# Kernel tuning notes

Hardware: AMD Instinct MI355X
Metric: run time of the kernel (lower is better)

## Reference

```python
import jax, jax.numpy as jnp
import numpy as np

N = 4096
IN_DIM = 256
OUT_DIM = 256
NUM_HEADS = 4
HEAD_DIM = OUT_DIM // NUM_HEADS


def setup_inputs() -> dict:
    key = jax.random.key(0)
    ks = jax.random.split(key, 10)
    x = jax.random.normal(ks[0], (N, IN_DIM), dtype=jnp.float32)
    adj = jax.random.randint(ks[1], (N, N), 0, 2, dtype=jnp.int32)
    adj = jnp.maximum(adj, jnp.eye(N, dtype=jnp.int32))  # self-loops -> no empty rows
    s_in = 1.0 / np.sqrt(IN_DIM)
    s_out = 1.0 / np.sqrt(OUT_DIM)
    Wq = jax.random.uniform(ks[2], (IN_DIM, OUT_DIM), jnp.float32, -s_in, s_in)
    bq = jnp.zeros((OUT_DIM,), jnp.float32)
    Wk = jax.random.uniform(ks[3], (IN_DIM, OUT_DIM), jnp.float32, -s_in, s_in)
    bk = jnp.zeros((OUT_DIM,), jnp.float32)
    Wv = jax.random.uniform(ks[4], (IN_DIM, OUT_DIM), jnp.float32, -s_in, s_in)
    bv = jnp.zeros((OUT_DIM,), jnp.float32)
    Wo = jax.random.uniform(ks[5], (OUT_DIM, OUT_DIM), jnp.float32, -s_out, s_out)
    bo = jnp.zeros((OUT_DIM,), jnp.float32)
    gamma = jnp.ones((OUT_DIM,), jnp.float32)
    beta = jnp.zeros((OUT_DIM,), jnp.float32)
    return {"x": x, "adj": adj, "Wq": Wq, "bq": bq, "Wk": Wk, "bk": bk,
            "Wv": Wv, "bv": bv, "Wo": Wo, "bo": bo, "gamma": gamma, "beta": beta}


def layer_norm(h, gamma, beta, eps=1e-5):
    mu = jnp.mean(h, axis=-1, keepdims=True)
    var = jnp.mean(jnp.square(h - mu), axis=-1, keepdims=True)
    return (h - mu) * jax.lax.rsqrt(var + eps) * gamma + beta


def reference(x, adj, Wq, bq, Wk, bk, Wv, bv, Wo, bo, gamma, beta):
    n = x.shape[0]
    q_proj = x @ Wq + bq                       # (N, out_dim), reused for residual
    Q = q_proj.reshape(n, NUM_HEADS, HEAD_DIM)
    K = (x @ Wk + bk).reshape(n, NUM_HEADS, HEAD_DIM)
    V = (x @ Wv + bv).reshape(n, NUM_HEADS, HEAD_DIM)
    scores = jnp.einsum('nhd,mhd->nmh', Q, K) / np.sqrt(HEAD_DIM)
    scores = jnp.where(adj[:, :, None] == 0, -jnp.inf, scores)
    attn = jax.nn.softmax(scores, axis=1)      # softmax over neighbor axis m
    out = jnp.einsum('nmh,mhd->nhd', attn, V).reshape(n, OUT_DIM)
    out = out @ Wo + bo
    return layer_norm(out + q_proj, gamma, beta)
```

## Files before the change

kernel.cpp:

```cpp
#include <hip/hip_runtime.h>
#include <math.h>

#define NN 4096
#define DIM 256
#define NHEADS 4
#define HDIM 64

typedef short bf16x8 __attribute__((ext_vector_type(8)));
typedef float f32x4  __attribute__((ext_vector_type(4)));

__device__ __forceinline__ unsigned short f2bf(float f) {
    unsigned int u = __float_as_uint(f);
    u += 0x7fffu + ((u >> 16) & 1u);
    return (unsigned short)(u >> 16);
}
__device__ __forceinline__ float bf2f(unsigned short h) {
    return __uint_as_float(((unsigned int)h) << 16);
}
__device__ __forceinline__ void async16(const void* g, void* l) {
    __builtin_amdgcn_global_load_lds(
        (const __attribute__((address_space(1))) unsigned int*)g,
        (__attribute__((address_space(3))) unsigned int*)l, 16, 0, 0);
}

__global__ __launch_bounds__(256)
void prep_kernel(const float* __restrict__ W0, const float* __restrict__ W1,
                 const float* __restrict__ W2, const float* __restrict__ W3,
                 unsigned short* __restrict__ T0, unsigned short* __restrict__ T1,
                 unsigned short* __restrict__ T2, unsigned short* __restrict__ T3)
{
    __shared__ unsigned short Ts[64][65];
    const int b = blockIdx.x, t = threadIdx.x;
    const int mat = b >> 4, tile = b & 15;
    const int r0 = (tile >> 2) * 64, c0 = (tile & 3) * 64;
    const float* W = (mat == 0) ? W0 : (mat == 1) ? W1 : (mat == 2) ? W2 : W3;
    unsigned short* T = (mat == 0) ? T0 : (mat == 1) ? T1 : (mat == 2) ? T2 : T3;
    {
        int r = t >> 2, c4 = (t & 3) * 16;
        #pragma unroll
        for (int j = 0; j < 4; ++j) {
            float4 v = *reinterpret_cast<const float4*>(W + (size_t)(r0 + r) * DIM + c0 + c4 + j * 4);
            Ts[c4 + j * 4 + 0][r] = f2bf(v.x);
            Ts[c4 + j * 4 + 1][r] = f2bf(v.y);
            Ts[c4 + j * 4 + 2][r] = f2bf(v.z);
            Ts[c4 + j * 4 + 3][r] = f2bf(v.w);
        }
    }
    __syncthreads();
    {
        int d = t >> 2, k4 = (t & 3) * 16;
        #pragma unroll
        for (int j = 0; j < 4; ++j) {
            ushort4 u;
            u.x = Ts[d][k4 + j * 4 + 0];
            u.y = Ts[d][k4 + j * 4 + 1];
            u.z = Ts[d][k4 + j * 4 + 2];
            u.w = Ts[d][k4 + j * 4 + 3];
            *reinterpret_cast<ushort4*>(T + (size_t)(c0 + d) * DIM + r0 + k4 + j * 4) = u;
        }
    }
}

__global__ __launch_bounds__(256)
void qkv_mask(const float* __restrict__ x,
              const unsigned short* __restrict__ WqT, const unsigned short* __restrict__ WkT,
              const unsigned short* __restrict__ WvT,
              const float* __restrict__ bq, const float* __restrict__ bk, const float* __restrict__ bv,
              unsigned short* __restrict__ Qo, unsigned short* __restrict__ Ko,
              unsigned short* __restrict__ VTo,
              const int* __restrict__ adj, unsigned long long* __restrict__ maskT)
{
    const int b = blockIdx.x, t = threadIdx.x, w = t >> 6, l = t & 63;

    if (b >= 384) {
        const int ww = (b - 384) * 4 + w;
        for (int idx = ww; idx < 65536; idx += 8192) {
            const int row = idx >> 4, st = idx & 15;
            const int4 a = *reinterpret_cast<const int4*>(adj + (size_t)row * NN + st * 256 + l * 4);
            unsigned long long b0 = __ballot(a.x != 0);
            unsigned long long b1 = __ballot(a.y != 0);
            unsigned long long b2 = __ballot(a.z != 0);
            unsigned long long b3 = __ballot(a.w != 0);
            if (l < 4) {
                unsigned long long bb = (l == 0) ? b0 : (l == 1) ? b1 : (l == 2) ? b2 : b3;
                maskT[(size_t)row * 64 + st * 4 + l] = bb;
            }
        }
        return;
    }

    const int l15 = l & 15, lg = l >> 4;
    const int which = b >> 7, xb = b & 127;
    const int row0 = xb * 32 + (w >> 1) * 16;
    const int col0 = (w & 1) * 128;
    const unsigned short* WT; const float* bias;
    if (which == 0)      { WT = WqT; bias = bq; }
    else if (which == 1) { WT = WkT; bias = bk; }
    else                 { WT = WvT; bias = bv; }

    f32x4 acc[8] = {};
    for (int k0 = 0; k0 < DIM; k0 += 32) {
        const float* xp = x + (size_t)(row0 + l15) * DIM + k0 + lg * 8;
        float4 x0 = *reinterpret_cast<const float4*>(xp);
        float4 x1 = *reinterpret_cast<const float4*>(xp + 4);
        union { unsigned u[4]; bf16x8 v; } xa;
        asm("v_cvt_pk_bf16_f32 %0, %1, %2" : "=v"(xa.u[0]) : "v"(x0.x), "v"(x0.y));
        asm("v_cvt_pk_bf16_f32 %0, %1, %2" : "=v"(xa.u[1]) : "v"(x0.z), "v"(x0.w));
        asm("v_cvt_pk_bf16_f32 %0, %1, %2" : "=v"(xa.u[2]) : "v"(x1.x), "v"(x1.y));
        asm("v_cvt_pk_bf16_f32 %0, %1, %2" : "=v"(xa.u[3]) : "v"(x1.z), "v"(x1.w));
        #pragma unroll
        for (int nt = 0; nt < 8; ++nt) {
            bf16x8 wb = *(const bf16x8*)(WT + (size_t)(col0 + nt * 16 + l15) * DIM + k0 + lg * 8);
            acc[nt] = __builtin_amdgcn_mfma_f32_16x16x32_bf16(xa.v, wb, acc[nt], 0, 0, 0);
        }
    }
    #pragma unroll
    for (int nt = 0; nt < 8; ++nt) {
        int col = col0 + nt * 16 + l15;
        float bb = bias[col];
        #pragma unroll
        for (int r = 0; r < 4; ++r) {
            int row = row0 + lg * 4 + r;
            unsigned short val = f2bf(acc[nt][r] + bb);
            if (which == 2) {
                int rb = row & 63;
                int vnt = rb >> 4, vlg = (rb >> 2) & 3, vr = rb & 3;
                int pos = ((vnt & 1) << 5) | (vlg << 3) | ((vnt >> 1) << 2) | vr;
                VTo[(size_t)col * NN + ((row & ~63) | pos)] = val;
            } else if (which == 0) Qo[(size_t)row * DIM + col] = val;
            else                   Ko[(size_t)row * DIM + col] = val;
        }
    }
}

template<int NTILES>
__global__ __launch_bounds__(256)
void attn_mfma(const unsigned short* __restrict__ Qb, const unsigned short* __restrict__ Kb,
               const unsigned short* __restrict__ VT, const unsigned long long* __restrict__ maskT,
               unsigned short* __restrict__ Opart, float* __restrict__ lpart)
{
    constexpr int NSTR = NTILES / 4;
    __shared__ unsigned short Kt[2][64][64];
    __shared__ unsigned short Vt[2][64][64];

    const int t = threadIdx.x, w = t >> 6, l = t & 63, l15 = l & 15, lg = l >> 4;
    const int n0 = blockIdx.x * 128, h = blockIdx.y, sp = blockIdx.z;
    const int kv_base = sp * NTILES * 64;
    const int qbase = n0 + w * 32;

    bf16x8 qa[2][2];
    #pragma unroll
    for (int sub = 0; sub < 2; ++sub) {
        const unsigned short* qp = Qb + (size_t)(qbase + sub * 16 + l15) * DIM + h * HDIM + lg * 8;
        qa[sub][0] = *(const bf16x8*)(qp);
        qa[sub][1] = *(const bf16x8*)(qp + 32);
    }

    const unsigned long long* mbase0 = maskT + (size_t)(qbase + l15) * 64 + (kv_base >> 6);
    const unsigned long long* mbase1 = maskT + (size_t)(qbase + 16 + l15) * 64 + (kv_base >> 6);

    const int srow  = w * 16 + (l >> 3);
    const int sunit = (l & 7) ^ (srow & 7);
    const unsigned short* kS = Kb + (size_t)(kv_base + srow) * DIM + h * HDIM + sunit * 8;
    const unsigned short* vS = VT + (size_t)(h * HDIM + srow) * NN + kv_base + sunit * 8;

    const int xr  = l15 & 7;
    const int ko0 = (lg ^ xr) << 4;
    const int ko1 = ((4 + lg) ^ xr) << 4;

    f32x4 oa[2][4] = {};
    float lsum[2] = {0.f, 0.f};

    {
        unsigned short* kd = &Kt[0][w * 16][0];
        unsigned short* vd = &Vt[0][w * 16][0];
        async16(kS,           kd);
        async16(kS + 8 * DIM, kd + 8 * 64);
        async16(vS,           vd);
        async16(vS + 8 * NN,  vd + 8 * 64);
    }

    #pragma unroll
    for (int st = 0; st < NSTR; ++st) {
        ulonglong4 m40 = *reinterpret_cast<const ulonglong4*>(mbase0 + st * 4);
        ulonglong4 m41 = *reinterpret_cast<const ulonglong4*>(mbase1 + st * 4);
        unsigned lo[2][4], hi[2][4];
        lo[0][0] = (unsigned)m40.x; hi[0][0] = (unsigned)(m40.x >> 32);
        lo[0][1] = (unsigned)m40.y; hi[0][1] = (unsigned)(m40.y >> 32);
        lo[0][2] = (unsigned)m40.z; hi[0][2] = (unsigned)(m40.z >> 32);
        lo[0][3] = (unsigned)m40.w; hi[0][3] = (unsigned)(m40.w >> 32);
        lo[1][0] = (unsigned)m41.x; hi[1][0] = (unsigned)(m41.x >> 32);
        lo[1][1] = (unsigned)m41.y; hi[1][1] = (unsigned)(m41.y >> 32);
        lo[1][2] = (unsigned)m41.z; hi[1][2] = (unsigned)(m41.z >> 32);
        lo[1][3] = (unsigned)m41.w; hi[1][3] = (unsigned)(m41.w >> 32);

        #pragma unroll
        for (int m = 0; m < 4; ++m) {
            const int tl = st * 4 + m;
            const int bsel = tl & 1;
            if (tl + 1 < NTILES) {
                const unsigned short* ks = kS + (size_t)(tl + 1) * 64 * DIM;
                const unsigned short* vs = vS + (tl + 1) * 64;
                unsigned short* kd = &Kt[bsel ^ 1][w * 16][0];
                unsigned short* vd = &Vt[bsel ^ 1][w * 16][0];
                async16(ks,           kd);
                async16(ks + 8 * DIM, kd + 8 * 64);
                async16(vs,           vd);
                async16(vs + 8 * NN,  vd + 8 * 64);
                asm volatile("s_waitcnt vmcnt(4)" ::: "memory");
            } else {
                asm volatile("s_waitcnt vmcnt(0)" ::: "memory");
            }
            __builtin_amdgcn_s_barrier();
            __builtin_amdgcn_sched_barrier(0);

            const char* kbase = (const char*)&Kt[bsel][0][0] + l15 * 128;
            const char* vbase = (const char*)&Vt[bsel][0][0] + l15 * 128;

            f32x4 sa[2][4] = {};
            __builtin_amdgcn_s_setprio(1);
            #pragma unroll
            for (int nt = 0; nt < 4; ++nt) {
                bf16x8 kb0 = *(const bf16x8*)(kbase + nt * 2048 + ko0);
                bf16x8 kb1 = *(const bf16x8*)(kbase + nt * 2048 + ko1);
                #pragma unroll
                for (int sub = 0; sub < 2; ++sub) {
                    sa[sub][nt] = __builtin_amdgcn_mfma_f32_16x16x32_bf16(kb0, qa[sub][0], sa[sub][nt], 0, 0, 0);
                    sa[sub][nt] = __builtin_amdgcn_mfma_f32_16x16x32_bf16(kb1, qa[sub][1], sa[sub][nt], 0, 0, 0);
                }
            }
            __builtin_amdgcn_s_setprio(0);

            const int bsh = ((m & 1) << 4) + lg;
            bf16x8 pa[2][2];
            #pragma unroll
            for (int sub = 0; sub < 2; ++sub) {
                unsigned s0 = ((m & 2) ? hi[sub][0] : lo[sub][0]) >> bsh;
                unsigned s1 = ((m & 2) ? hi[sub][1] : lo[sub][1]) >> bsh;
                unsigned s2 = ((m & 2) ? hi[sub][2] : lo[sub][2]) >> bsh;
                unsigned s3 = ((m & 2) ? hi[sub][3] : lo[sub][3]) >> bsh;
                float p[4][4];
                #pragma unroll
                for (int nt = 0; nt < 4; ++nt) {
                    p[nt][0] = exp2f(((s0 >> (nt * 4)) & 1u) ? sa[sub][nt][0] * 0.18033688f : -INFINITY);
                    p[nt][1] = exp2f(((s1 >> (nt * 4)) & 1u) ? sa[sub][nt][1] * 0.18033688f : -INFINITY);
                    p[nt][2] = exp2f(((s2 >> (nt * 4)) & 1u) ? sa[sub][nt][2] * 0.18033688f : -INFINITY);
                    p[nt][3] = exp2f(((s3 >> (nt * 4)) & 1u) ? sa[sub][nt][3] * 0.18033688f : -INFINITY);
                }
                lsum[sub] += (((p[0][0] + p[0][1]) + (p[0][2] + p[0][3])) +
                              ((p[1][0] + p[1][1]) + (p[1][2] + p[1][3]))) +
                             (((p[2][0] + p[2][1]) + (p[2][2] + p[2][3])) +
                              ((p[3][0] + p[3][1]) + (p[3][2] + p[3][3])));
                union { unsigned u[4]; bf16x8 v; } a0, a1;
                asm("v_cvt_pk_bf16_f32 %0, %1, %2" : "=v"(a0.u[0]) : "v"(p[0][0]), "v"(p[0][1]));
                asm("v_cvt_pk_bf16_f32 %0, %1, %2" : "=v"(a0.u[1]) : "v"(p[0][2]), "v"(p[0][3]));
                asm("v_cvt_pk_bf16_f32 %0, %1, %2" : "=v"(a0.u[2]) : "v"(p[2][0]), "v"(p[2][1]));
                asm("v_cvt_pk_bf16_f32 %0, %1, %2" : "=v"(a0.u[3]) : "v"(p[2][2]), "v"(p[2][3]));
                asm("v_cvt_pk_bf16_f32 %0, %1, %2" : "=v"(a1.u[0]) : "v"(p[1][0]), "v"(p[1][1]));
                asm("v_cvt_pk_bf16_f32 %0, %1, %2" : "=v"(a1.u[1]) : "v"(p[1][2]), "v"(p[1][3]));
                asm("v_cvt_pk_bf16_f32 %0, %1, %2" : "=v"(a1.u[2]) : "v"(p[3][0]), "v"(p[3][1]));
                asm("v_cvt_pk_bf16_f32 %0, %1, %2" : "=v"(a1.u[3]) : "v"(p[3][2]), "v"(p[3][3]));
                pa[sub][0] = a0.v;
                pa[sub][1] = a1.v;
            }

            __builtin_amdgcn_s_setprio(1);
            #pragma unroll
            for (int nt = 0; nt < 4; ++nt) {
                bf16x8 vb0 = *(const bf16x8*)(vbase + nt * 2048 + ko0);
                bf16x8 vb1 = *(const bf16x8*)(vbase + nt * 2048 + ko1);
                #pragma unroll
                for (int sub = 0; sub < 2; ++sub) {
                    oa[sub][nt] = __builtin_amdgcn_mfma_f32_16x16x32_bf16(pa[sub][0], vb0, oa[sub][nt], 0, 0, 0);
                    oa[sub][nt] = __builtin_amdgcn_mfma_f32_16x16x32_bf16(pa[sub][1], vb1, oa[sub][nt], 0, 0, 0);
                }
            }
            __builtin_amdgcn_s_setprio(0);

            __builtin_amdgcn_sched_barrier(0);
            __builtin_amdgcn_s_barrier();
        }
    }

    #pragma unroll
    for (int sub = 0; sub < 2; ++sub) {
        float v = lsum[sub];
        v += __shfl_xor(v, 16);
        v += __shfl_xor(v, 32);
        if (lg == 0)
            lpart[((size_t)sp * NN + qbase + sub * 16 + l15) * NHEADS + h] = v;
        #pragma unroll
        for (int r = 0; r < 4; ++r) {
            const int qr = qbase + sub * 16 + lg * 4 + r;
            #pragma unroll
            for (int nt = 0; nt < 4; ++nt)
                Opart[((size_t)sp * NN + qr) * DIM + h * HDIM + nt * 16 + l15] = f2bf(oa[sub][nt][r]);
        }
    }
}

__global__ __launch_bounds__(256)
void combine_kernel(const unsigned short* __restrict__ Opart, const float* __restrict__ lpart,
                    unsigned short* __restrict__ AOb, int S)
{
    const int tid = blockIdx.x * blockDim.x + threadIdx.x;
    const int q  = tid >> 6;
    const int d  = (tid & 63) * 4;
    const int h  = d >> 6;
    float o0 = 0.f, o1 = 0.f, o2 = 0.f, o3 = 0.f, lsum = 0.f;
    for (int s = 0; s < S; ++s) {
        ushort4 u = *reinterpret_cast<const ushort4*>(Opart + ((size_t)s * NN + q) * DIM + d);
        o0 += bf2f(u.x); o1 += bf2f(u.y); o2 += bf2f(u.z); o3 += bf2f(u.w);
        lsum += lpart[((size_t)s * NN + q) * NHEADS + h];
    }
    float inv = 1.f / lsum;
    ushort4 o;
    o.x = f2bf(o0 * inv); o.y = f2bf(o1 * inv); o.z = f2bf(o2 * inv); o.w = f2bf(o3 * inv);
    *reinterpret_cast<ushort4*>(AOb + (size_t)q * DIM + d) = o;
}

__global__ __launch_bounds__(256)
void out_ln(const unsigned short* __restrict__ Ab, const unsigned short* __restrict__ WoT,
            const float* __restrict__ bo, const unsigned short* __restrict__ Rb,
            const float* __restrict__ gamma, const float* __restrict__ beta,
            float* __restrict__ out)
{
    __shared__ float redsum[4][16];
    __shared__ float redsq[4][16];
    const int t = threadIdx.x, w = t >> 6, l = t & 63, l15 = l & 15, lg = l >> 4;
    const int row0 = blockIdx.x * 16;
    const int col0 = w * 64;

    f32x4 acc[4] = {};
    for (int k0 = 0; k0 < DIM; k0 += 32) {
        bf16x8 xa = *(const bf16x8*)(Ab + (size_t)(row0 + l15) * DIM + k0 + lg * 8);
        #pragma unroll
        for (int nt = 0; nt < 4; ++nt) {
            bf16x8 wb = *(const bf16x8*)(WoT + (size_t)(col0 + nt * 16 + l15) * DIM + k0 + lg * 8);
            acc[nt] = __builtin_amdgcn_mfma_f32_16x16x32_bf16(xa, wb, acc[nt], 0, 0, 0);
        }
    }

    float psum[4] = {0, 0, 0, 0}, psq[4] = {0, 0, 0, 0};
    #pragma unroll
    for (int nt = 0; nt < 4; ++nt) {
        int col = col0 + nt * 16 + l15;
        float bb = bo[col];
        #pragma unroll
        for (int r = 0; r < 4; ++r) {
            int row = row0 + lg * 4 + r;
            float xv = acc[nt][r] + bb + bf2f(Rb[(size_t)row * DIM + col]);
            acc[nt][r] = xv;
            psum[r] += xv; psq[r] += xv * xv;
        }
    }
    #pragma unroll
    for (int r = 0; r < 4; ++r) {
        float s = psum[r], q = psq[r];
        s += __shfl_xor(s, 1); q += __shfl_xor(q, 1);
        s += __shfl_xor(s, 2); q += __shfl_xor(q, 2);
        s += __shfl_xor(s, 4); q += __shfl_xor(q, 4);
        s += __shfl_xor(s, 8); q += __shfl_xor(q, 8);
        psum[r] = s; psq[r] = q;
    }
    if (l15 == 0) {
        #pragma unroll
        for (int r = 0; r < 4; ++r) {
            redsum[w][lg * 4 + r] = psum[r];
            redsq[w][lg * 4 + r]  = psq[r];
        }
    }
    __syncthreads();

    float msave[4], rsave[4];
    #pragma unroll
    for (int r = 0; r < 4; ++r) {
        int row = lg * 4 + r;
        float s = redsum[0][row] + redsum[1][row] + redsum[2][row] + redsum[3][row];
        float q = redsq[0][row] + redsq[1][row] + redsq[2][row] + redsq[3][row];
        float mean = s * (1.f / 256.f);
        float var  = q * (1.f / 256.f) - mean * mean;
        msave[r] = mean;
        rsave[r] = rsqrtf(var + 1e-5f);
    }
    #pragma unroll
    for (int nt = 0; nt < 4; ++nt) {
        int col = col0 + nt * 16 + l15;
        float g = gamma[col], bt = beta[col];
        #pragma unroll
        for (int r = 0; r < 4; ++r) {
            int row = row0 + lg * 4 + r;
            out[(size_t)row * DIM + col] = (acc[nt][r] - msave[r]) * rsave[r] * g + bt;
        }
    }
}

extern "C" void kernel_launch(void* const* d_in, const int* in_sizes, int n_in,
                              void* d_out, int out_size, void* d_ws, size_t ws_size,
                              hipStream_t stream) {
    const float* x     = (const float*)d_in[0];
    const int*   adj   = (const int*)  d_in[1];
    const float* Wq    = (const float*)d_in[2];
    const float* bq    = (const float*)d_in[3];
    const float* Wk    = (const float*)d_in[4];
    const float* bk    = (const float*)d_in[5];
    const float* Wv    = (const float*)d_in[6];
    const float* bv    = (const float*)d_in[7];
    const float* Wo    = (const float*)d_in[8];
    const float* bo    = (const float*)d_in[9];
    const float* gamma = (const float*)d_in[10];
    const float* beta  = (const float*)d_in[11];
    float* out = (float*)d_out;

    char* ws = (char*)d_ws;
    const size_t MB = 1u << 20;
    unsigned short*     Qb    = (unsigned short*)(ws + 0 * MB);
    unsigned short*     Kb    = (unsigned short*)(ws + 2 * MB);
    unsigned short*     VT    = (unsigned short*)(ws + 4 * MB);
    unsigned long long* maskT = (unsigned long long*)(ws + 6 * MB);
    unsigned short*     WqT   = (unsigned short*)(ws + 8 * MB);
    unsigned short*     WkT   = (unsigned short*)(ws + 8 * MB + 128 * 1024);
    unsigned short*     WvT   = (unsigned short*)(ws + 8 * MB + 256 * 1024);
    unsigned short*     WoT   = (unsigned short*)(ws + 8 * MB + 384 * 1024);
    unsigned short*     AOb   = (unsigned short*)(ws + 8 * MB + 512 * 1024);
    float*              lpart = (float*)(ws + 10 * MB + 512 * 1024);
    unsigned short*     Opart = (unsigned short*)(ws + 11 * MB);

    const int S = (ws_size >= 27 * MB) ? 8 : 4;

    prep_kernel<<<64, 256, 0, stream>>>(Wq, Wk, Wv, Wo, WqT, WkT, WvT, WoT);

    qkv_mask<<<384 + 2048, 256, 0, stream>>>(
        x, WqT, WkT, WvT, bq, bk, bv, Qb, Kb, VT, adj, maskT);

    if (S == 8)
        attn_mfma<8><<<dim3(NN / 128, NHEADS, 8), 256, 0, stream>>>(
            Qb, Kb, VT, maskT, Opart, lpart);
    else
        attn_mfma<16><<<dim3(NN / 128, NHEADS, 4), 256, 0, stream>>>(
            Qb, Kb, VT, maskT, Opart, lpart);

    combine_kernel<<<NN * DIM / 4 / 256, 256, 0, stream>>>(Opart, lpart, AOb, S);

    out_ln<<<NN / 16, 256, 0, stream>>>(AOb, WoT, bo, Qb, gamma, beta, out);
}
```

Baseline: 90.74 us.

## Triple-buffer K/V tiles, halve query rows per block, prescale K

The attention kernel moves from double to triple buffering of K/V tiles in LDS. Prefetch now runs two tiles ahead, with one barrier per tile instead of two. Each wave handles 16 query rows instead of 32, so the grid doubles and register pressure drops, but each block reuses fewer loaded K/V tiles and global K/V traffic doubles. The softmax scale is folded into K when it is stored in the projection kernel, which removes a multiply per score.

```diff
diff --git a/kernel.cpp b/kernel.cpp
--- a/kernel.cpp
+++ b/kernel.cpp
@@ -121,7 +121,9 @@
         #pragma unroll
         for (int r = 0; r < 4; ++r) {
             int row = row0 + lg * 4 + r;
-            unsigned short val = f2bf(acc[nt][r] + bb);
+            float ov = acc[nt][r] + bb;
+            if (which == 1) ov *= 0.18033688f;
+            unsigned short val = f2bf(ov);
             if (which == 2) {
                 int rb = row & 63;
                 int vnt = rb >> 4, vlg = (rb >> 2) & 3, vr = rb & 3;
@@ -140,24 +142,19 @@
                unsigned short* __restrict__ Opart, float* __restrict__ lpart)
 {
     constexpr int NSTR = NTILES / 4;
-    __shared__ unsigned short Kt[2][64][64];
-    __shared__ unsigned short Vt[2][64][64];
+    __shared__ unsigned short Kt[3][64][64];
+    __shared__ unsigned short Vt[3][64][64];
 
     const int t = threadIdx.x, w = t >> 6, l = t & 63, l15 = l & 15, lg = l >> 4;
-    const int n0 = blockIdx.x * 128, h = blockIdx.y, sp = blockIdx.z;
+    const int n0 = blockIdx.x * 64, h = blockIdx.y, sp = blockIdx.z;
     const int kv_base = sp * NTILES * 64;
-    const int qbase = n0 + w * 32;
-
-    bf16x8 qa[2][2];
-    #pragma unroll
-    for (int sub = 0; sub < 2; ++sub) {
-        const unsigned short* qp = Qb + (size_t)(qbase + sub * 16 + l15) * DIM + h * HDIM + lg * 8;
-        qa[sub][0] = *(const bf16x8*)(qp);
-        qa[sub][1] = *(const bf16x8*)(qp + 32);
-    }
-
-    const unsigned long long* mbase0 = maskT + (size_t)(qbase + l15) * 64 + (kv_base >> 6);
-    const unsigned long long* mbase1 = maskT + (size_t)(qbase + 16 + l15) * 64 + (kv_base >> 6);
+    const int qrow = n0 + w * 16;
+
+    const unsigned short* qp = Qb + (size_t)(qrow + l15) * DIM + h * HDIM + lg * 8;
+    const bf16x8 qa0 = *(const bf16x8*)(qp);
+    const bf16x8 qa1 = *(const bf16x8*)(qp + 32);
+
+    const unsigned long long* mbase = maskT + (size_t)(qrow + l15) * 64 + (kv_base >> 6);
 
     const int srow  = w * 16 + (l >> 3);
     const int sunit = (l & 7) ^ (srow & 7);
@@ -168,134 +165,113 @@
     const int ko0 = (lg ^ xr) << 4;
     const int ko1 = ((4 + lg) ^ xr) << 4;
 
-    f32x4 oa[2][4] = {};
-    float lsum[2] = {0.f, 0.f};
-
-    {
-        unsigned short* kd = &Kt[0][w * 16][0];
-        unsigned short* vd = &Vt[0][w * 16][0];
-        async16(kS,           kd);
-        async16(kS + 8 * DIM, kd + 8 * 64);
-        async16(vS,           vd);
-        async16(vS + 8 * NN,  vd + 8 * 64);
+    f32x4 oa[4] = {};
+    float lsum = 0.f;
+
+    #pragma unroll
+    for (int pt = 0; pt < 2; ++pt) {
+        unsigned short* kd = &Kt[pt][w * 16][0];
+        unsigned short* vd = &Vt[pt][w * 16][0];
+        const unsigned short* ks = kS + (size_t)pt * 64 * DIM;
+        const unsigned short* vs = vS + pt * 64;
+        async16(ks, kd); async16(ks + 8 * DIM, kd + 8 * 64);
+        async16(vs, vd); async16(vs + 8 * NN,  vd + 8 * 64);
     }
 
     #pragma unroll
     for (int st = 0; st < NSTR; ++st) {
-        ulonglong4 m40 = *reinterpret_cast<const ulonglong4*>(mbase0 + st * 4);
-        ulonglong4 m41 = *reinterpret_cast<const ulonglong4*>(mbase1 + st * 4);
-        unsigned lo[2][4], hi[2][4];
-        lo[0][0] = (unsigned)m40.x; hi[0][0] = (unsigned)(m40.x >> 32);
-        lo[0][1] = (unsigned)m40.y; hi[0][1] = (unsigned)(m40.y >> 32);
-        lo[0][2] = (unsigned)m40.z; hi[0][2] = (unsigned)(m40.z >> 32);
-        lo[0][3] = (unsigned)m40.w; hi[0][3] = (unsigned)(m40.w >> 32);
-        lo[1][0] = (unsigned)m41.x; hi[1][0] = (unsigned)(m41.x >> 32);
-        lo[1][1] = (unsigned)m41.y; hi[1][1] = (unsigned)(m41.y >> 32);
-        lo[1][2] = (unsigned)m41.z; hi[1][2] = (unsigned)(m41.z >> 32);
-        lo[1][3] = (unsigned)m41.w; hi[1][3] = (unsigned)(m41.w >> 32);
+        const ulonglong4 m4 = *reinterpret_cast<const ulonglong4*>(mbase + st * 4);
+        const unsigned lo[4] = {(unsigned)m4.x, (unsigned)m4.y, (unsigned)m4.z, (unsigned)m4.w};
+        const unsigned hi[4] = {(unsigned)(m4.x >> 32), (unsigned)(m4.y >> 32),
+                                (unsigned)(m4.z >> 32), (unsigned)(m4.w >> 32)};
 
         #pragma unroll
         for (int m = 0; m < 4; ++m) {
             const int tl = st * 4 + m;
-            const int bsel = tl & 1;
-            if (tl + 1 < NTILES) {
-                const unsigned short* ks = kS + (size_t)(tl + 1) * 64 * DIM;
-                const unsigned short* vs = vS + (tl + 1) * 64;
-                unsigned short* kd = &Kt[bsel ^ 1][w * 16][0];
-                unsigned short* vd = &Vt[bsel ^ 1][w * 16][0];
-                async16(ks,           kd);
-                async16(ks + 8 * DIM, kd + 8 * 64);
-                async16(vs,           vd);
-                async16(vs + 8 * NN,  vd + 8 * 64);
-                asm volatile("s_waitcnt vmcnt(4)" ::: "memory");
-            } else {
-                asm volatile("s_waitcnt vmcnt(0)" ::: "memory");
-            }
+            if (tl < NTILES - 1) asm volatile("s_waitcnt vmcnt(4)" ::: "memory");
+            else                 asm volatile("s_waitcnt vmcnt(0)" ::: "memory");
             __builtin_amdgcn_s_barrier();
             __builtin_amdgcn_sched_barrier(0);
 
-            const char* kbase = (const char*)&Kt[bsel][0][0] + l15 * 128;
-            const char* vbase = (const char*)&Vt[bsel][0][0] + l15 * 128;
-
-            f32x4 sa[2][4] = {};
+            if (tl + 2 < NTILES) {
+                const int bb = (tl + 2) % 3;
+                unsigned short* kd = &Kt[bb][w * 16][0];
+                unsigned short* vd = &Vt[bb][w * 16][0];
+                const unsigned short* ks = kS + (size_t)(tl + 2) * 64 * DIM;
+                const unsigned short* vs = vS + (tl + 2) * 64;
+                async16(ks, kd); async16(ks + 8 * DIM, kd + 8 * 64);
+                async16(vs, vd); async16(vs + 8 * NN,  vd + 8 * 64);
+            }
+
+            const int cb = tl % 3;
+            const char* kbase = (const char*)&Kt[cb][0][0] + l15 * 128;
+            const char* vbase = (const char*)&Vt[cb][0][0] + l15 * 128;
+
+            f32x4 sa[4] = {};
             __builtin_amdgcn_s_setprio(1);
             #pragma unroll
             for (int nt = 0; nt < 4; ++nt) {
                 bf16x8 kb0 = *(const bf16x8*)(kbase + nt * 2048 + ko0);
                 bf16x8 kb1 = *(const bf16x8*)(kbase + nt * 2048 + ko1);
-                #pragma unroll
-                for (int sub = 0; sub < 2; ++sub) {
-                    sa[sub][nt] = __builtin_amdgcn_mfma_f32_16x16x32_bf16(kb0, qa[sub][0], sa[sub][nt], 0, 0, 0);
-                    sa[sub][nt] = __builtin_amdgcn_mfma_f32_16x16x32_bf16(kb1, qa[sub][1], sa[sub][nt], 0, 0, 0);
-                }
+                sa[nt] = __builtin_amdgcn_mfma_f32_16x16x32_bf16(kb0, qa0, sa[nt], 0, 0, 0);
+                sa[nt] = __builtin_amdgcn_mfma_f32_16x16x32_bf16(kb1, qa1, sa[nt], 0, 0, 0);
             }
             __builtin_amdgcn_s_setprio(0);
 
             const int bsh = ((m & 1) << 4) + lg;
-            bf16x8 pa[2][2];
+            const unsigned s0 = ((m & 2) ? hi[0] : lo[0]) >> bsh;
+            const unsigned s1 = ((m & 2) ? hi[1] : lo[1]) >> bsh;
+            const unsigned s2 = ((m & 2) ? hi[2] : lo[2]) >> bsh;
+            const unsigned s3 = ((m & 2) ? hi[3] : lo[3]) >> bsh;
+            float p[4][4];
             #pragma unroll
-            for (int sub = 0; sub < 2; ++sub) {
-                unsigned s0 = ((m & 2) ? hi[sub][0] : lo[sub][0]) >> bsh;
-                unsigned s1 = ((m & 2) ? hi[sub][1] : lo[sub][1]) >> bsh;
-                unsigned s2 = ((m & 2) ? hi[sub][2] : lo[sub][2]) >> bsh;
-                unsigned s3 = ((m & 2) ? hi[sub][3] : lo[sub][3]) >> bsh;
-                float p[4][4];
-                #pragma unroll
-                for (int nt = 0; nt < 4; ++nt) {
-                    p[nt][0] = exp2f(((s0 >> (nt * 4)) & 1u) ? sa[sub][nt][0] * 0.18033688f : -INFINITY);
-                    p[nt][1] = exp2f(((s1 >> (nt * 4)) & 1u) ? sa[sub][nt][1] * 0.18033688f : -INFINITY);
-                    p[nt][2] = exp2f(((s2 >> (nt * 4)) & 1u) ? sa[sub][nt][2] * 0.18033688f : -INFINITY);
-                    p[nt][3] = exp2f(((s3 >> (nt * 4)) & 1u) ? sa[sub][nt][3] * 0.18033688f : -INFINITY);
-                }
-                lsum[sub] += (((p[0][0] + p[0][1]) + (p[0][2] + p[0][3])) +
-                              ((p[1][0] + p[1][1]) + (p[1][2] + p[1][3]))) +
-                             (((p[2][0] + p[2][1]) + (p[2][2] + p[2][3])) +
-                              ((p[3][0] + p[3][1]) + (p[3][2] + p[3][3])));
-                union { unsigned u[4]; bf16x8 v; } a0, a1;
-                asm("v_cvt_pk_bf16_f32 %0, %1, %2" : "=v"(a0.u[0]) : "v"(p[0][0]), "v"(p[0][1]));
-                asm("v_cvt_pk_bf16_f32 %0, %1, %2" : "=v"(a0.u[1]) : "v"(p[0][2]), "v"(p[0][3]));
-                asm("v_cvt_pk_bf16_f32 %0, %1, %2" : "=v"(a0.u[2]) : "v"(p[2][0]), "v"(p[2][1]));
-                asm("v_cvt_pk_bf16_f32 %0, %1, %2" : "=v"(a0.u[3]) : "v"(p[2][2]), "v"(p[2][3]));
-                asm("v_cvt_pk_bf16_f32 %0, %1, %2" : "=v"(a1.u[0]) : "v"(p[1][0]), "v"(p[1][1]));
-                asm("v_cvt_pk_bf16_f32 %0, %1, %2" : "=v"(a1.u[1]) : "v"(p[1][2]), "v"(p[1][3]));
-                asm("v_cvt_pk_bf16_f32 %0, %1, %2" : "=v"(a1.u[2]) : "v"(p[3][0]), "v"(p[3][1]));
-                asm("v_cvt_pk_bf16_f32 %0, %1, %2" : "=v"(a1.u[3]) : "v"(p[3][2]), "v"(p[3][3]));
-                pa[sub][0] = a0.v;
-                pa[sub][1] = a1.v;
+            for (int nt = 0; nt < 4; ++nt) {
+                p[nt][0] = exp2f(((s0 >> (nt * 4)) & 1u) ? sa[nt][0] : -INFINITY);
+                p[nt][1] = exp2f(((s1 >> (nt * 4)) & 1u) ? sa[nt][1] : -INFINITY);
+                p[nt][2] = exp2f(((s2 >> (nt * 4)) & 1u) ? sa[nt][2] : -INFINITY);
+                p[nt][3] = exp2f(((s3 >> (nt * 4)) & 1u) ? sa[nt][3] : -INFINITY);
             }
+            lsum += (((p[0][0] + p[0][1]) + (p[0][2] + p[0][3])) +
+                     ((p[1][0] + p[1][1]) + (p[1][2] + p[1][3]))) +
+                    (((p[2][0] + p[2][1]) + (p[2][2] + p[2][3])) +
+                     ((p[3][0] + p[3][1]) + (p[3][2] + p[3][3])));
+            union { unsigned u[4]; bf16x8 v; } a0, a1;
+            asm("v_cvt_pk_bf16_f32 %0, %1, %2" : "=v"(a0.u[0]) : "v"(p[0][0]), "v"(p[0][1]));
+            asm("v_cvt_pk_bf16_f32 %0, %1, %2" : "=v"(a0.u[1]) : "v"(p[0][2]), "v"(p[0][3]));
+            asm("v_cvt_pk_bf16_f32 %0, %1, %2" : "=v"(a0.u[2]) : "v"(p[2][0]), "v"(p[2][1]));
+            asm("v_cvt_pk_bf16_f32 %0, %1, %2" : "=v"(a0.u[3]) : "v"(p[2][2]), "v"(p[2][3]));
+            asm("v_cvt_pk_bf16_f32 %0, %1, %2" : "=v"(a1.u[0]) : "v"(p[1][0]), "v"(p[1][1]));
+            asm("v_cvt_pk_bf16_f32 %0, %1, %2" : "=v"(a1.u[1]) : "v"(p[1][2]), "v"(p[1][3]));
+            asm("v_cvt_pk_bf16_f32 %0, %1, %2" : "=v"(a1.u[2]) : "v"(p[3][0]), "v"(p[3][1]));
+            asm("v_cvt_pk_bf16_f32 %0, %1, %2" : "=v"(a1.u[3]) : "v"(p[3][2]), "v"(p[3][3]));
+            const bf16x8 pa0 = a0.v;
+            const bf16x8 pa1 = a1.v;
 
             __builtin_amdgcn_s_setprio(1);
             #pragma unroll
             for (int nt = 0; nt < 4; ++nt) {
                 bf16x8 vb0 = *(const bf16x8*)(vbase + nt * 2048 + ko0);
                 bf16x8 vb1 = *(const bf16x8*)(vbase + nt * 2048 + ko1);
-                #pragma unroll
-                for (int sub = 0; sub < 2; ++sub) {
-                    oa[sub][nt] = __builtin_amdgcn_mfma_f32_16x16x32_bf16(pa[sub][0], vb0, oa[sub][nt], 0, 0, 0);
-                    oa[sub][nt] = __builtin_amdgcn_mfma_f32_16x16x32_bf16(pa[sub][1], vb1, oa[sub][nt], 0, 0, 0);
-                }
+                oa[nt] = __builtin_amdgcn_mfma_f32_16x16x32_bf16(pa0, vb0, oa[nt], 0, 0, 0);
+                oa[nt] = __builtin_amdgcn_mfma_f32_16x16x32_bf16(pa1, vb1, oa[nt], 0, 0, 0);
             }
             __builtin_amdgcn_s_setprio(0);
-
-            __builtin_amdgcn_sched_barrier(0);
-            __builtin_amdgcn_s_barrier();
-        }
-    }
-
-    #pragma unroll
-    for (int sub = 0; sub < 2; ++sub) {
-        float v = lsum[sub];
+        }
+    }
+
+    {
+        float v = lsum;
         v += __shfl_xor(v, 16);
         v += __shfl_xor(v, 32);
         if (lg == 0)
-            lpart[((size_t)sp * NN + qbase + sub * 16 + l15) * NHEADS + h] = v;
-        #pragma unroll
-        for (int r = 0; r < 4; ++r) {
-            const int qr = qbase + sub * 16 + lg * 4 + r;
-            #pragma unroll
-            for (int nt = 0; nt < 4; ++nt)
-                Opart[((size_t)sp * NN + qr) * DIM + h * HDIM + nt * 16 + l15] = f2bf(oa[sub][nt][r]);
-        }
+            lpart[((size_t)sp * NN + qrow + l15) * NHEADS + h] = v;
+    }
+    #pragma unroll
+    for (int r = 0; r < 4; ++r) {
+        const int qr = qrow + lg * 4 + r;
+        #pragma unroll
+        for (int nt = 0; nt < 4; ++nt)
+            Opart[((size_t)sp * NN + qr) * DIM + h * HDIM + nt * 16 + l15] = f2bf(oa[nt][r]);
     }
 }
 
@@ -434,10 +410,10 @@
         x, WqT, WkT, WvT, bq, bk, bv, Qb, Kb, VT, adj, maskT);
 
     if (S == 8)
-        attn_mfma<8><<<dim3(NN / 128, NHEADS, 8), 256, 0, stream>>>(
+        attn_mfma<8><<<dim3(NN / 64, NHEADS, 8), 256, 0, stream>>>(
             Qb, Kb, VT, maskT, Opart, lpart);
     else
-        attn_mfma<16><<<dim3(NN / 128, NHEADS, 4), 256, 0, stream>>>(
+        attn_mfma<16><<<dim3(NN / 64, NHEADS, 4), 256, 0, stream>>>(
             Qb, Kb, VT, maskT, Opart, lpart);
 
     combine_kernel<<<NN * DIM / 4 / 256, 256, 0, stream>>>(Opart, lpart, AOb, S);
```

Result: faster. 88.27 us (-2.7%).
